# Optimization experiments

Measured on AMD Instinct MI355X. Metric: run time of the kernel, lower is better.

The kernel has to match this reference:

```python
import jax, jax.numpy as jnp
import numpy as np

D_MODEL = 2048
N_Q = 32
N_KV = 8
HEAD_DIM = D_MODEL // N_Q  # 64
N_REP = N_Q // N_KV        # 4
QKV_OUT = HEAD_DIM * (N_Q + 2 * N_KV)  # 3072


def setup_inputs() -> dict:
    key = jax.random.key(0)
    ks = jax.random.split(key, 6)
    s = 1.0 / np.sqrt(D_MODEL)
    x = jax.random.normal(ks[0], (2, 2048, D_MODEL), dtype=jnp.float32)
    Wqkv = jax.random.normal(ks[1], (D_MODEL, QKV_OUT), dtype=jnp.float32) * s
    bqkv = jax.random.normal(ks[2], (QKV_OUT,), dtype=jnp.float32) * 0.02
    Wo = jax.random.normal(ks[3], (D_MODEL, D_MODEL), dtype=jnp.float32) * s
    bo = jax.random.normal(ks[4], (D_MODEL,), dtype=jnp.float32) * 0.02
    return {"x": x, "Wqkv": Wqkv, "bqkv": bqkv, "Wo": Wo, "bo": bo}


def reference(x, Wqkv, bqkv, Wo, bo):
    bsz, seqlen, _ = x.shape
    qkv = jnp.einsum('bsd,df->bsf', x, Wqkv) + bqkv
    q_end = HEAD_DIM * N_Q
    k_end = q_end + HEAD_DIM * N_KV
    q = qkv[..., :q_end].reshape(bsz, seqlen, N_Q, HEAD_DIM)
    k = qkv[..., q_end:k_end].reshape(bsz, seqlen, N_KV, HEAD_DIM)
    v = qkv[..., k_end:].reshape(bsz, seqlen, N_KV, HEAD_DIM)
    # GQA expansion: repeat kv heads n_rep times -> [b, s, N_Q, hd]
    k = jnp.repeat(k, N_REP, axis=2)
    v = jnp.repeat(v, N_REP, axis=2)
    # scores [b, h, s, s]
    scores = jnp.einsum('bqhd,bkhd->bhqk', q, k) / np.sqrt(HEAD_DIM).astype(np.float32)
    attn = jax.nn.softmax(scores, axis=-1)
    out = jnp.einsum('bhqk,bkhd->bqhd', attn, v).reshape(bsz, seqlen, D_MODEL)
    return jnp.einsum('bsd,de->bse', out, Wo) + bo
```

## Files before the change

### kernel.cpp

```cpp
#include <hip/hip_runtime.h>
#include <stdint.h>

typedef __attribute__((ext_vector_type(8))) __bf16 bf16x8;
typedef __attribute__((ext_vector_type(4))) float f32x4;
typedef uint16_t u16;
typedef __attribute__((address_space(1))) uint32_t ga_u32;
typedef __attribute__((address_space(3))) uint32_t lds_u32;

#define MFMA16(a, b, c) __builtin_amdgcn_mfma_f32_16x16x32_bf16(a, b, c, 0, 0, 0)

static __device__ __forceinline__ u16 f2bf(float f) {
  uint32_t u = __float_as_uint(f);
  u += 0x7FFFu + ((u >> 16) & 1u);
  return (u16)(u >> 16);
}

static __device__ __forceinline__ void async_cp16(const void* src, void* dst) {
  __builtin_amdgcn_global_load_lds((ga_u32*)src, (lds_u32*)dst, 16, 0, 0);
}

__global__ void cast_bf16_kernel(const float* __restrict__ in, u16* __restrict__ out, int n4) {
  int i = blockIdx.x * 256 + threadIdx.x;
  if (i < n4) {
    float4 v = reinterpret_cast<const float4*>(in)[i];
    ushort4 o;
    o.x = f2bf(v.x); o.y = f2bf(v.y); o.z = f2bf(v.z); o.w = f2bf(v.w);
    reinterpret_cast<ushort4*>(out)[i] = o;
  }
}

__global__ void transpose_cast_kernel(const float* __restrict__ W, u16* __restrict__ WT,
                                      int K, int N) {
  __shared__ float tile[32][33];
  int tx = threadIdx.x & 31, ty = threadIdx.x >> 5;
  int n0 = blockIdx.x * 32, k0 = blockIdx.y * 32;
#pragma unroll
  for (int i = 0; i < 32; i += 8)
    tile[ty + i][tx] = W[(size_t)(k0 + ty + i) * N + n0 + tx];
  __syncthreads();
#pragma unroll
  for (int i = 0; i < 32; i += 8)
    WT[(size_t)(n0 + ty + i) * K + k0 + tx] = f2bf(tile[tx][ty + i]);
}

template <int MODE>
__global__ void gemm_bt_kernel(const u16* __restrict__ A, const u16* __restrict__ BT,
                               const float* __restrict__ bias, void* __restrict__ C,
                               u16* __restrict__ vT,
                               int M, int N, int K, int OUTN) {
  __shared__ __align__(16) u16 sA[2][128 * 32];
  __shared__ __align__(16) u16 sB[2][128 * 32];
  int tid = threadIdx.x, lane = tid & 63, wave = tid >> 6;
  int wm = wave >> 1, wn = wave & 1;
  int row0 = blockIdx.y * 128, col0 = blockIdx.x * 128;
  int l15 = lane & 15, l4 = lane >> 4;

  int srow = wave * 32 + (lane >> 2);
  int sslot = (((lane & 3) ^ ((srow >> 1) & 3))) * 8;
  auto stage = [&](const u16* g, int r0, int k0, u16* lds) {
#pragma unroll
    for (int j = 0; j < 2; ++j) {
      const u16* src = g + (size_t)(r0 + srow + j * 16) * K + k0 + sslot;
      async_cp16(src, lds + (wave * 2 + j) * 512);
    }
  };

  f32x4 acc[4][4] = {};
  stage(A, row0, 0, sA[0]);
  stage(BT, col0, 0, sB[0]);
  __syncthreads();
  int nk = K >> 5, cur = 0;
  for (int kt = 0; kt < nk; ++kt) {
    if (kt + 1 < nk) {
      stage(A, row0, (kt + 1) * 32, sA[cur ^ 1]);
      stage(BT, col0, (kt + 1) * 32, sB[cur ^ 1]);
    }
    bf16x8 af[4], bfr[4];
#pragma unroll
    for (int m = 0; m < 4; ++m) {
      int ra = wm * 64 + m * 16 + l15;
      af[m] = *reinterpret_cast<const bf16x8*>(&sA[cur][ra * 32 + ((l4 ^ ((ra >> 1) & 3)) & 3) * 8]);
    }
#pragma unroll
    for (int n = 0; n < 4; ++n) {
      int rb = wn * 64 + n * 16 + l15;
      bfr[n] = *reinterpret_cast<const bf16x8*>(&sB[cur][rb * 32 + ((l4 ^ ((rb >> 1) & 3)) & 3) * 8]);
    }
#pragma unroll
    for (int m = 0; m < 4; ++m)
#pragma unroll
      for (int n = 0; n < 4; ++n)
        acc[m][n] = MFMA16(af[m], bfr[n], acc[m][n]);
    __syncthreads();
    cur ^= 1;
  }

  bool vpart = (MODE == 1) && (col0 >= 2560);
#pragma unroll
  for (int m = 0; m < 4; ++m) {
#pragma unroll
    for (int n = 0; n < 4; ++n) {
      int col = col0 + wn * 64 + n * 16 + l15;
      float bv = bias[col];
      int rowb = row0 + wm * 64 + m * 16 + l4 * 4;
      if (vpart) {
        int hk = (col - 2560) >> 6, d = col & 63;
        int b = rowb >> 11, s = rowb & 2047;
        ushort4 o;
        o.x = f2bf(acc[m][n][0] + bv); o.y = f2bf(acc[m][n][1] + bv);
        o.z = f2bf(acc[m][n][2] + bv); o.w = f2bf(acc[m][n][3] + bv);
        *reinterpret_cast<ushort4*>(&vT[((size_t)((b * 8 + hk) * 64 + d)) * 2048 + s]) = o;
      } else {
#pragma unroll
        for (int e = 0; e < 4; ++e) {
          float v = acc[m][n][e] + bv;
          if (MODE == 1)
            ((u16*)C)[(size_t)(rowb + e) * OUTN + col] = f2bf(v);
          else
            ((float*)C)[(size_t)(rowb + e) * OUTN + col] = v;
        }
      }
    }
  }
}

__global__ __launch_bounds__(256, 3)
void attn_kernel(const u16* __restrict__ qkv, const u16* __restrict__ vTg,
                 u16* __restrict__ attno) {
  __shared__ __align__(16) u16 Kl[2][64 * 64];
  __shared__ __align__(16) u16 Vl[2][64 * 64];
  __shared__ __align__(16) u16 Pw[4][32 * 72];

  int qt = blockIdx.x, bh = blockIdx.y;
  int b = bh >> 5, h = bh & 31, g = h >> 2;
  int tid = threadIdx.x, lane = tid & 63, w = tid >> 6;
  int l15 = lane & 15, l4 = lane >> 4;
  size_t rowbase = (size_t)b * 2048;

  bf16x8 aq[2][2];
#pragma unroll
  for (int mf = 0; mf < 2; ++mf)
#pragma unroll
    for (int ks = 0; ks < 2; ++ks)
      aq[mf][ks] = *reinterpret_cast<const bf16x8*>(
          qkv + (rowbase + qt * 128 + w * 32 + mf * 16 + l15) * 2560 + h * 64 + ks * 32 + l4 * 8);

  int src_r = lane >> 3;
  int sslot = ((lane & 7) ^ src_r) * 8;
  const u16* Kg = qkv + rowbase * 2560 + 2048 + g * 64;
  const u16* Vg = vTg + ((size_t)((b * 8 + g) * 64)) * 2048;

  auto stageKV = [&](int kt, int buf) {
#pragma unroll
    for (int j = 0; j < 2; ++j) {
      int c = w * 2 + j;
      async_cp16(Kg + (size_t)(kt * 64 + c * 8 + src_r) * 2560 + sslot, &Kl[buf][c * 512]);
    }
#pragma unroll
    for (int j = 0; j < 2; ++j) {
      int c = w * 2 + j;
      async_cp16(Vg + (size_t)(c * 8 + src_r) * 2048 + kt * 64 + sslot, &Vl[buf][c * 512]);
    }
  };

  f32x4 oacc[2][4] = {};
  f32x4 lacc[2] = {};
  union { short s[8]; bf16x8 v; } ones;
#pragma unroll
  for (int i = 0; i < 8; ++i) ones.s[i] = 0x3F80;

  stageKV(0, 0);
  const float CEXP = 0.18033688011112042f;

  for (int kt = 0; kt < 32; ++kt) {
    int cur = kt & 1;
    __syncthreads();
    if (kt + 1 < 32) stageKV(kt + 1, cur ^ 1);

    f32x4 s[2][4] = {};
#pragma unroll
    for (int ks = 0; ks < 2; ++ks) {
      bf16x8 bk[4];
#pragma unroll
      for (int nf = 0; nf < 4; ++nf) {
        int key = nf * 16 + l15;
        bk[nf] = *reinterpret_cast<const bf16x8*>(
            &Kl[cur][key * 64 + (((ks * 4 + l4) ^ (key & 7)) * 8)]);
      }
#pragma unroll
      for (int mf = 0; mf < 2; ++mf)
#pragma unroll
        for (int nf = 0; nf < 4; ++nf)
          s[mf][nf] = MFMA16(aq[mf][ks], bk[nf], s[mf][nf]);
    }

#pragma unroll
    for (int mf = 0; mf < 2; ++mf)
#pragma unroll
      for (int nf = 0; nf < 4; ++nf)
#pragma unroll
        for (int e = 0; e < 4; ++e)
          Pw[w][(mf * 16 + l4 * 4 + e) * 72 + nf * 16 + l15] =
              f2bf(__builtin_amdgcn_exp2f(s[mf][nf][e] * CEXP));

#pragma unroll
    for (int ks = 0; ks < 2; ++ks) {
      bf16x8 pa[2], bv[4];
#pragma unroll
      for (int mf = 0; mf < 2; ++mf)
        pa[mf] = *reinterpret_cast<const bf16x8*>(&Pw[w][(mf * 16 + l15) * 72 + ks * 32 + l4 * 8]);
#pragma unroll
      for (int df = 0; df < 4; ++df) {
        int d = df * 16 + l15;
        bv[df] = *reinterpret_cast<const bf16x8*>(
            &Vl[cur][d * 64 + (((ks * 4 + l4) ^ (d & 7)) * 8)]);
      }
#pragma unroll
      for (int mf = 0; mf < 2; ++mf) {
        lacc[mf] = MFMA16(pa[mf], ones.v, lacc[mf]);
#pragma unroll
        for (int df = 0; df < 4; ++df)
          oacc[mf][df] = MFMA16(pa[mf], bv[df], oacc[mf][df]);
      }
    }
  }

#pragma unroll
  for (int mf = 0; mf < 2; ++mf)
#pragma unroll
    for (int df = 0; df < 4; ++df) {
      int col = h * 64 + df * 16 + l15;
#pragma unroll
      for (int e = 0; e < 4; ++e) {
        size_t row = rowbase + qt * 128 + w * 32 + mf * 16 + l4 * 4 + e;
        attno[row * 2048 + col] = f2bf(oacc[mf][df][e] / lacc[mf][e]);
      }
    }
}

extern "C" void kernel_launch(void* const* d_in, const int* in_sizes, int n_in,
                              void* d_out, int out_size, void* d_ws, size_t ws_size,
                              hipStream_t stream) {
  const float* x    = (const float*)d_in[0];
  const float* Wqkv = (const float*)d_in[1];
  const float* bqkv = (const float*)d_in[2];
  const float* Wo   = (const float*)d_in[3];
  const float* bo   = (const float*)d_in[4];
  float* out = (float*)d_out;

  char* ws = (char*)d_ws;
  u16* x_bf   = (u16*)(ws);
  u16* WqkvT  = (u16*)(ws + 16777216);
  u16* WoT    = (u16*)(ws + 29360128);
  u16* qkv_bf = (u16*)(ws + 37748736);
  u16* attno  = (u16*)(ws + 58720256);
  u16* vT     = (u16*)(ws + 75497472);

  cast_bf16_kernel<<<8192, 256, 0, stream>>>(x, x_bf, 2097152);
  transpose_cast_kernel<<<dim3(96, 64), 256, 0, stream>>>(Wqkv, WqkvT, 2048, 3072);
  transpose_cast_kernel<<<dim3(64, 64), 256, 0, stream>>>(Wo, WoT, 2048, 2048);
  gemm_bt_kernel<1><<<dim3(24, 32), 256, 0, stream>>>(x_bf, WqkvT, bqkv, qkv_bf, vT,
                                                      4096, 3072, 2048, 2560);
  attn_kernel<<<dim3(16, 64), 256, 0, stream>>>(qkv_bf, vT, attno);
  gemm_bt_kernel<0><<<dim3(16, 32), 256, 0, stream>>>(attno, WoT, bo, out, nullptr,
                                                      4096, 2048, 2048, 2048);
}
```

Baseline: 328.4 us.

## Swizzle workgroups across XCDs and transpose score MFMA for packed P stores

Remaps 1D grids so consecutive workgroups landing on the same XCD share GEMM/attention tiles for better L2 locality. In attention, the QK^T MFMA operands are swapped so each lane holds consecutive keys, allowing packed 8-byte stores of P into a compact XOR-swizzled LDS buffer instead of scalar stores to a padded one. The P·V stage is interleaved per 32-key chunk, and the occupancy hint is raised to 4 blocks per CU, which may increase register pressure or spilling.

```diff
diff --git a/kernel.cpp b/kernel.cpp
--- a/kernel.cpp
+++ b/kernel.cpp
@@ -47,12 +47,15 @@
 __global__ void gemm_bt_kernel(const u16* __restrict__ A, const u16* __restrict__ BT,
                                const float* __restrict__ bias, void* __restrict__ C,
                                u16* __restrict__ vT,
-                               int M, int N, int K, int OUTN) {
+                               int NBX, int N, int K, int OUTN) {
   __shared__ __align__(16) u16 sA[2][128 * 32];
   __shared__ __align__(16) u16 sB[2][128 * 32];
   int tid = threadIdx.x, lane = tid & 63, wave = tid >> 6;
   int wm = wave >> 1, wn = wave & 1;
-  int row0 = blockIdx.y * 128, col0 = blockIdx.x * 128;
+  int nwg = gridDim.x, wid = blockIdx.x;
+  int swz = (wid & 7) * (nwg >> 3) + (wid >> 3);
+  int by = swz / NBX, bx = swz - by * NBX;
+  int row0 = by * 128, col0 = bx * 128;
   int l15 = lane & 15, l4 = lane >> 4;
 
   int srow = wave * 32 + (lane >> 2);
@@ -124,14 +127,16 @@
   }
 }
 
-__global__ __launch_bounds__(256, 3)
+__global__ __launch_bounds__(256, 4)
 void attn_kernel(const u16* __restrict__ qkv, const u16* __restrict__ vTg,
                  u16* __restrict__ attno) {
   __shared__ __align__(16) u16 Kl[2][64 * 64];
   __shared__ __align__(16) u16 Vl[2][64 * 64];
-  __shared__ __align__(16) u16 Pw[4][32 * 72];
-
-  int qt = blockIdx.x, bh = blockIdx.y;
+  __shared__ __align__(16) u16 Pw[4][1024];
+
+  int wid = blockIdx.x;
+  int swz = (wid & 7) * 128 + (wid >> 3);
+  int qt = swz & 15, bh = swz >> 4;
   int b = bh >> 5, h = bh & 31, g = h >> 2;
   int tid = threadIdx.x, lane = tid & 63, w = tid >> 6;
   int l15 = lane & 15, l4 = lane >> 4;
@@ -139,11 +144,11 @@
 
   bf16x8 aq[2][2];
 #pragma unroll
-  for (int mf = 0; mf < 2; ++mf)
+  for (int qf = 0; qf < 2; ++qf)
 #pragma unroll
     for (int ks = 0; ks < 2; ++ks)
-      aq[mf][ks] = *reinterpret_cast<const bf16x8*>(
-          qkv + (rowbase + qt * 128 + w * 32 + mf * 16 + l15) * 2560 + h * 64 + ks * 32 + l4 * 8);
+      aq[qf][ks] = *reinterpret_cast<const bf16x8*>(
+          qkv + (rowbase + qt * 128 + w * 32 + qf * 16 + l15) * 2560 + h * 64 + ks * 32 + l4 * 8);
 
   int src_r = lane >> 3;
   int sslot = ((lane & 7) ^ src_r) * 8;
@@ -171,6 +176,7 @@
 
   stageKV(0, 0);
   const float CEXP = 0.18033688011112042f;
+  char* pwb = (char*)&Pw[w][0];
 
   for (int kt = 0; kt < 32; ++kt) {
     int cur = kt & 1;
@@ -182,58 +188,74 @@
     for (int ks = 0; ks < 2; ++ks) {
       bf16x8 bk[4];
 #pragma unroll
-      for (int nf = 0; nf < 4; ++nf) {
-        int key = nf * 16 + l15;
-        bk[nf] = *reinterpret_cast<const bf16x8*>(
+      for (int kf = 0; kf < 4; ++kf) {
+        int key = kf * 16 + l15;
+        bk[kf] = *reinterpret_cast<const bf16x8*>(
             &Kl[cur][key * 64 + (((ks * 4 + l4) ^ (key & 7)) * 8)]);
       }
 #pragma unroll
-      for (int mf = 0; mf < 2; ++mf)
-#pragma unroll
-        for (int nf = 0; nf < 4; ++nf)
-          s[mf][nf] = MFMA16(aq[mf][ks], bk[nf], s[mf][nf]);
-    }
-
-#pragma unroll
-    for (int mf = 0; mf < 2; ++mf)
-#pragma unroll
-      for (int nf = 0; nf < 4; ++nf)
+      for (int qf = 0; qf < 2; ++qf)
+#pragma unroll
+        for (int kf = 0; kf < 4; ++kf)
+          s[qf][kf] = MFMA16(bk[kf], aq[qf][ks], s[qf][kf]);
+    }
+
+#pragma unroll
+    for (int qf = 0; qf < 2; ++qf)
+#pragma unroll
+      for (int kf = 0; kf < 4; ++kf)
 #pragma unroll
         for (int e = 0; e < 4; ++e)
-          Pw[w][(mf * 16 + l4 * 4 + e) * 72 + nf * 16 + l15] =
-              f2bf(__builtin_amdgcn_exp2f(s[mf][nf][e] * CEXP));
-
-#pragma unroll
-    for (int ks = 0; ks < 2; ++ks) {
+          s[qf][kf][e] = __builtin_amdgcn_exp2f(s[qf][kf][e] * CEXP);
+
+#pragma unroll
+    for (int kc = 0; kc < 2; ++kc) {
+#pragma unroll
+      for (int qf = 0; qf < 2; ++qf) {
+        int ql = qf * 16 + l15;
+#pragma unroll
+        for (int kh = 0; kh < 2; ++kh) {
+          union { ushort4 u; __bf16 bb[4]; } pk;
+#pragma unroll
+          for (int e = 0; e < 4; ++e) pk.bb[e] = (__bf16)s[qf][kc * 2 + kh][e];
+          int off = ((ql << 6) + (kh << 5) + (l4 << 3)) ^ ((ql & 3) << 4);
+          *reinterpret_cast<ushort4*>(pwb + off) = pk.u;
+        }
+      }
+      asm volatile("" ::: "memory");
       bf16x8 pa[2], bv[4];
 #pragma unroll
-      for (int mf = 0; mf < 2; ++mf)
-        pa[mf] = *reinterpret_cast<const bf16x8*>(&Pw[w][(mf * 16 + l15) * 72 + ks * 32 + l4 * 8]);
+      for (int qf = 0; qf < 2; ++qf) {
+        int ql = qf * 16 + l15;
+        int off = ((ql << 6) + (l4 << 4)) ^ ((ql & 3) << 4);
+        pa[qf] = *reinterpret_cast<const bf16x8*>(pwb + off);
+      }
 #pragma unroll
       for (int df = 0; df < 4; ++df) {
         int d = df * 16 + l15;
         bv[df] = *reinterpret_cast<const bf16x8*>(
-            &Vl[cur][d * 64 + (((ks * 4 + l4) ^ (d & 7)) * 8)]);
-      }
-#pragma unroll
-      for (int mf = 0; mf < 2; ++mf) {
-        lacc[mf] = MFMA16(pa[mf], ones.v, lacc[mf]);
+            &Vl[cur][d * 64 + (((kc * 4 + l4) ^ (d & 7)) * 8)]);
+      }
+#pragma unroll
+      for (int qf = 0; qf < 2; ++qf) {
+        lacc[qf] = MFMA16(pa[qf], ones.v, lacc[qf]);
 #pragma unroll
         for (int df = 0; df < 4; ++df)
-          oacc[mf][df] = MFMA16(pa[mf], bv[df], oacc[mf][df]);
-      }
-    }
-  }
-
-#pragma unroll
-  for (int mf = 0; mf < 2; ++mf)
+          oacc[qf][df] = MFMA16(pa[qf], bv[df], oacc[qf][df]);
+      }
+      asm volatile("" ::: "memory");
+    }
+  }
+
+#pragma unroll
+  for (int qf = 0; qf < 2; ++qf)
 #pragma unroll
     for (int df = 0; df < 4; ++df) {
       int col = h * 64 + df * 16 + l15;
 #pragma unroll
       for (int e = 0; e < 4; ++e) {
-        size_t row = rowbase + qt * 128 + w * 32 + mf * 16 + l4 * 4 + e;
-        attno[row * 2048 + col] = f2bf(oacc[mf][df][e] / lacc[mf][e]);
+        size_t row = rowbase + qt * 128 + w * 32 + qf * 16 + l4 * 4 + e;
+        attno[row * 2048 + col] = f2bf(oacc[qf][df][e] / lacc[qf][e]);
       }
     }
 }
@@ -259,9 +281,9 @@
   cast_bf16_kernel<<<8192, 256, 0, stream>>>(x, x_bf, 2097152);
   transpose_cast_kernel<<<dim3(96, 64), 256, 0, stream>>>(Wqkv, WqkvT, 2048, 3072);
   transpose_cast_kernel<<<dim3(64, 64), 256, 0, stream>>>(Wo, WoT, 2048, 2048);
-  gemm_bt_kernel<1><<<dim3(24, 32), 256, 0, stream>>>(x_bf, WqkvT, bqkv, qkv_bf, vT,
-                                                      4096, 3072, 2048, 2560);
-  attn_kernel<<<dim3(16, 64), 256, 0, stream>>>(qkv_bf, vT, attno);
-  gemm_bt_kernel<0><<<dim3(16, 32), 256, 0, stream>>>(attno, WoT, bo, out, nullptr,
-                                                      4096, 2048, 2048, 2048);
-}
+  gemm_bt_kernel<1><<<768, 256, 0, stream>>>(x_bf, WqkvT, bqkv, qkv_bf, vT,
+                                             24, 3072, 2048, 2560);
+  attn_kernel<<<1024, 256, 0, stream>>>(qkv_bf, vT, attno);
+  gemm_bt_kernel<0><<<512, 256, 0, stream>>>(attno, WoT, bo, out, nullptr,
+                                             16, 2048, 2048, 2048);
+}
```

Result: faster. 314.9 us (-4.1%).
